# Performance work log

Hardware: AMD Instinct MI355X
Metric: run time of the kernel (lower is better)

The kernel has to match this reference:

```python
import jax, jax.numpy as jnp
import numpy as np

NUM_HEADS = 4
CHUNK = 64
GATE_NORM = 16.0
EPS = 1e-5


def _xavier(key, fan_in, fan_out):
    gain = 2.0 ** (-2.5)
    limit = gain * np.sqrt(6.0 / (fan_in + fan_out))
    return jax.random.uniform(key, (fan_in, fan_out), jnp.float32, -limit, limit)


def setup_inputs() -> dict:
    key = jax.random.key(0)
    ks = jax.random.split(key, 8)
    B, L, D = 4, 2048, 1024
    Dk, Dv, R = 1024, 2048, 16
    x = jax.random.normal(ks[0], (B, L, D), jnp.float32)
    return {
        "x": x,
        "Wq": _xavier(ks[1], D, Dk),
        "Wk": _xavier(ks[2], D, Dk),
        "Wv": _xavier(ks[3], D, Dv),
        "Wg": _xavier(ks[4], D, Dv),
        "gk_w1": _xavier(ks[5], D, R),
        "gk_w2": _xavier(ks[6], R, Dk),
        "gk_b2": jnp.zeros((Dk,), jnp.float32),
        "g_norm_w": jnp.ones((Dv // NUM_HEADS,), jnp.float32),
        "Wo": _xavier(ks[7], Dv, D),
    }


def _to_chunks(t, B, H, NC, C):
    # [B,H,L,d] -> [NC,B,H,C,d]
    d = t.shape[-1]
    return t.reshape(B, H, NC, C, d).transpose(2, 0, 1, 3, 4)


def _gla_forward(x, Wq, Wk, Wv, Wg, gk_w1, gk_w2, gk_b2, g_norm_w, Wo):
    B, L, D = x.shape
    H = NUM_HEADS
    C = CHUNK
    NC = L // C

    q = x @ Wq  # [B,L,Dk]
    k = x @ Wk
    v = x @ Wv  # [B,L,Dv]
    gk = jax.nn.log_sigmoid((x @ gk_w1) @ gk_w2 + gk_b2) / GATE_NORM  # [B,L,Dk]

    def split_heads(t):
        return t.reshape(B, L, H, -1).transpose(0, 2, 1, 3)  # [B,H,L,d]

    q, k, v, gk = map(split_heads, (q, k, v, gk))
    dk = q.shape[-1]
    scale = dk ** -0.5

    qc = _to_chunks(q, B, H, NC, C)
    kc = _to_chunks(k, B, H, NC, C)
    vc = _to_chunks(v, B, H, NC, C)
    gc = _to_chunks(gk, B, H, NC, C)
    Bcum = jnp.cumsum(gc, axis=3)  # inclusive log-decay within chunk

    causal = jnp.tril(jnp.ones((C, C), jnp.float32))  # s <= t

    def step(Hst, inp):
        qi, ki, vi, bi = inp  # [B,H,C,dk/dv]
        qg = qi * jnp.exp(bi) * scale           # q_t * exp(B_t)
        kg = ki * jnp.exp(-bi)                  # k_s * exp(-B_s)
        o_inter = jnp.einsum('bhcd,bhde->bhce', qg, Hst)
        A = jnp.einsum('bhtd,bhsd->bhts', qg, kg) * causal
        o_intra = jnp.einsum('bhts,bhse->bhte', A, vi)
        b_last = bi[:, :, -1:, :]               # total chunk decay [B,H,1,dk]
        kH = ki * jnp.exp(b_last - bi)          # decay remaining after s
        H_new = jnp.exp(b_last).transpose(0, 1, 3, 2) * Hst + \
            jnp.einsum('bhcd,bhce->bhde', kH, vi)
        return H_new, o_inter + o_intra

    dv = v.shape[-1]
    H0 = jnp.zeros((B, H, dk, dv), jnp.float32)
    _, oc = jax.lax.scan(step, H0, (qc, kc, vc, Bcum))  # [NC,B,H,C,dv]
    o = oc.transpose(1, 2, 0, 3, 4).reshape(B, H, L, dv)
    o = o.transpose(0, 2, 1, 3)  # [B,L,H,dv]

    # FusedRMSNormSwishGate: RMSNorm(o) * w * swish(g)
    rms = jnp.sqrt(jnp.mean(o * o, axis=-1, keepdims=True) + EPS)
    o_n = (o / rms) * g_norm_w
    g = (x @ Wg).reshape(B, L, H, dv)
    o = o_n * g * jax.nn.sigmoid(g)
    return o.reshape(B, L, H * dv) @ Wo


def reference(x, Wq, Wk, Wv, Wg, gk_w1, gk_w2, gk_b2, g_norm_w, Wo):
    return _gla_forward(x, Wq, Wk, Wv, Wg, gk_w1, gk_w2, gk_b2, g_norm_w, Wo)
```

## Files before the change

### kernel.cpp

```cpp
#include <hip/hip_runtime.h>
#include <hip/hip_bf16.h>

typedef __attribute__((ext_vector_type(8))) __bf16 bf16x8;
typedef __attribute__((ext_vector_type(4))) __bf16 bf16x4;
typedef __attribute__((ext_vector_type(4))) float f32x4;

#define MFMA16(a, b, c) __builtin_amdgcn_mfma_f32_16x16x32_bf16((a), (b), (c), 0, 0, 0)

__device__ __forceinline__ void gload_lds16(const void* g, void* l) {
    __builtin_amdgcn_global_load_lds((const __attribute__((address_space(1))) void*)g,
                                     (__attribute__((address_space(3))) void*)l, 16, 0, 0);
}

__device__ __forceinline__ int lds_swz(int r, int ck) {
    int W = ((r & 15) << 6) | (ck << 4);
    W ^= ((W >> 7) & 7) << 4;
    return ((r >> 4) << 9) + (W >> 1);
}

__global__ __launch_bounds__(256) void transpose_all(
    const float* __restrict__ Wq, const float* __restrict__ Wk,
    const float* __restrict__ Wg, const float* __restrict__ Wv,
    const float* __restrict__ Wo, __bf16* __restrict__ WTqk,
    __bf16* __restrict__ WTg, __bf16* __restrict__ WvT, __bf16* __restrict__ WoT) {
    __shared__ float tile[32][33];
    const int bid = blockIdx.x;
    const float* in;
    __bf16* out;
    int R, C, loc, gw;
    if (bid < 1024)      { in = Wq; out = WTqk;            R = 1024; C = 1024; loc = bid;        gw = 32; }
    else if (bid < 2048) { in = Wk; out = WTqk + 1048576;  R = 1024; C = 1024; loc = bid - 1024; gw = 32; }
    else if (bid < 4096) { in = Wg; out = WTg;             R = 1024; C = 2048; loc = bid - 2048; gw = 64; }
    else if (bid < 6144) { in = Wv; out = WvT;             R = 1024; C = 2048; loc = bid - 4096; gw = 64; }
    else                 { in = Wo; out = WoT;             R = 2048; C = 1024; loc = bid - 6144; gw = 32; }
    const int c0 = (loc % gw) * 32, r0 = (loc / gw) * 32;
    const int tx = threadIdx.x & 31, ty = threadIdx.x >> 5;
#pragma unroll
    for (int k = 0; k < 32; k += 8)
        tile[ty + k][tx] = in[(size_t)(r0 + ty + k) * C + c0 + tx];
    __syncthreads();
#pragma unroll
    for (int k = 0; k < 32; k += 8)
        out[(size_t)(c0 + ty + k) * R + r0 + tx] = (__bf16)tile[tx][ty + k];
}

template <typename OUT_T>
__global__ __launch_bounds__(256) void gemm_bt(const __bf16* __restrict__ A,
                                               const __bf16* __restrict__ Bt,
                                               OUT_T* __restrict__ C, int M, int N, int K) {
    __shared__ alignas(16) __bf16 As[2][4096];
    __shared__ alignas(16) __bf16 Bs[2][4096];
    const int tid = threadIdx.x;
    const int wv = tid >> 6;
    const int l = tid & 63;
    const int nwg = gridDim.x;
    const int cpx = nwg >> 3;
    const int bid = blockIdx.x;
    const int wg = (bid & 7) * cpx + (bid >> 3);
    const int nbn = N >> 7;
    const int bm = wg / nbn, bn = wg - bm * nbn;

    const __bf16* Ab = A + (size_t)bm * 128 * K;
    const __bf16* Bb = Bt + (size_t)bn * 128 * K;
    const int L = (l << 4) ^ ((l >> 3) << 4);
    const int sr = L >> 6;
    const int sc8 = ((L >> 4) & 3) * 8;
    const int lr = tid & 15;
    const int ck = (tid >> 4) & 3;
    const int wm = (wv >> 1) * 64, wn = (wv & 1) * 64;

    auto STAGE = [&](int buf, int kt) {
        gload_lds16(Ab + (size_t)(wv * 16 + sr) * K + kt + sc8, &As[buf][0] + wv * 512);
        gload_lds16(Ab + (size_t)(64 + wv * 16 + sr) * K + kt + sc8, &As[buf][0] + 2048 + wv * 512);
        gload_lds16(Bb + (size_t)(wv * 16 + sr) * K + kt + sc8, &Bs[buf][0] + wv * 512);
        gload_lds16(Bb + (size_t)(64 + wv * 16 + sr) * K + kt + sc8, &Bs[buf][0] + 2048 + wv * 512);
    };

    const int nt = K >> 5;
    STAGE(0, 0);

    f32x4 acc[4][4] = {};
    for (int t = 0; t < nt; ++t) {
        __builtin_amdgcn_s_barrier();
        __builtin_amdgcn_sched_barrier(0);
        if (t + 1 < nt) {
            STAGE((t + 1) & 1, (t + 1) * 32);
            asm volatile("s_waitcnt vmcnt(4)" ::: "memory");
        } else {
            asm volatile("s_waitcnt vmcnt(0)" ::: "memory");
        }
        __builtin_amdgcn_sched_barrier(0);
        const __bf16* as = &As[t & 1][0];
        const __bf16* bs = &Bs[t & 1][0];
        bf16x8 af[4], bfr[4];
#pragma unroll
        for (int i = 0; i < 4; i++) af[i] = *(const bf16x8*)(as + lds_swz(wm + i * 16 + lr, ck));
#pragma unroll
        for (int j = 0; j < 4; j++) bfr[j] = *(const bf16x8*)(bs + lds_swz(wn + j * 16 + lr, ck));
#pragma unroll
        for (int i = 0; i < 4; i++)
#pragma unroll
            for (int j = 0; j < 4; j++) acc[i][j] = MFMA16(af[i], bfr[j], acc[i][j]);
        asm volatile("s_waitcnt lgkmcnt(0)" ::: "memory");
    }
    const int lro = ((tid >> 4) & 3) * 4;
#pragma unroll
    for (int i = 0; i < 4; i++)
#pragma unroll
        for (int j = 0; j < 4; j++) {
            size_t base = (size_t)(bm * 128 + wm + i * 16 + lro) * N + bn * 128 + wn + j * 16 + lr;
#pragma unroll
            for (int r = 0; r < 4; r++) C[base + (size_t)r * N] = (OUT_T)acc[i][j][r];
        }
}

__global__ __launch_bounds__(256) void gemm_proj(const __bf16* __restrict__ xb,
                                                 const __bf16* __restrict__ WT,
                                                 const __bf16* __restrict__ WvT,
                                                 __bf16* __restrict__ Cq,
                                                 __bf16* __restrict__ Cg,
                                                 __bf16* __restrict__ vt) {
    constexpr int K = 1024;
    __shared__ alignas(16) __bf16 As[2][4096];
    __shared__ alignas(16) __bf16 Bs[2][4096];
    const int tid = threadIdx.x;
    const int wv = tid >> 6;
    const int l = tid & 63;
    const int bid = blockIdx.x;
    const int wg = (bid & 7) * 384 + (bid >> 3);
    const int mode = (wg >= 2048);
    int bm, bn;
    const __bf16 *Ab, *Bb;
    if (!mode) {
        bm = wg >> 5; bn = wg & 31;
        Ab = xb + (size_t)bm * 128 * K;
        Bb = WT + (size_t)bn * 128 * K;
    } else {
        const int w2 = wg - 2048;
        bm = w2 >> 6; bn = w2 & 63;
        Ab = WvT + (size_t)bm * 128 * K;
        Bb = xb + (size_t)bn * 128 * K;
    }
    const int L = (l << 4) ^ ((l >> 3) << 4);
    const int sr = L >> 6;
    const int sc8 = ((L >> 4) & 3) * 8;
    const int lr = tid & 15;
    const int ck = (tid >> 4) & 3;
    const int wm = (wv >> 1) * 64, wn = (wv & 1) * 64;

    auto STAGE = [&](int buf, int kt) {
        gload_lds16(Ab + (size_t)(wv * 16 + sr) * K + kt + sc8, &As[buf][0] + wv * 512);
        gload_lds16(Ab + (size_t)(64 + wv * 16 + sr) * K + kt + sc8, &As[buf][0] + 2048 + wv * 512);
        gload_lds16(Bb + (size_t)(wv * 16 + sr) * K + kt + sc8, &Bs[buf][0] + wv * 512);
        gload_lds16(Bb + (size_t)(64 + wv * 16 + sr) * K + kt + sc8, &Bs[buf][0] + 2048 + wv * 512);
    };

    const int nt = K >> 5;
    STAGE(0, 0);

    f32x4 acc[4][4] = {};
    for (int t = 0; t < nt; ++t) {
        __builtin_amdgcn_s_barrier();
        __builtin_amdgcn_sched_barrier(0);
        if (t + 1 < nt) {
            STAGE((t + 1) & 1, (t + 1) * 32);
            asm volatile("s_waitcnt vmcnt(4)" ::: "memory");
        } else {
            asm volatile("s_waitcnt vmcnt(0)" ::: "memory");
        }
        __builtin_amdgcn_sched_barrier(0);
        const __bf16* as = &As[t & 1][0];
        const __bf16* bs = &Bs[t & 1][0];
        bf16x8 af[4], bfr[4];
#pragma unroll
        for (int i = 0; i < 4; i++) af[i] = *(const bf16x8*)(as + lds_swz(wm + i * 16 + lr, ck));
#pragma unroll
        for (int j = 0; j < 4; j++) bfr[j] = *(const bf16x8*)(bs + lds_swz(wn + j * 16 + lr, ck));
#pragma unroll
        for (int i = 0; i < 4; i++)
#pragma unroll
            for (int j = 0; j < 4; j++) acc[i][j] = MFMA16(af[i], bfr[j], acc[i][j]);
        asm volatile("s_waitcnt lgkmcnt(0)" ::: "memory");
    }
    const int lro = ((tid >> 4) & 3) * 4;
    if (!mode) {
        __bf16* Cd = (bn < 16) ? Cq : Cg;
        const int col0 = (bn & 15) * 128;
#pragma unroll
        for (int i = 0; i < 4; i++)
#pragma unroll
            for (int j = 0; j < 4; j++) {
                size_t base = (size_t)(bm * 128 + wm + i * 16 + lro) * 2048 + col0 + wn + j * 16 + lr;
#pragma unroll
                for (int r = 0; r < 4; r++) Cd[base + (size_t)r * 2048] = (__bf16)acc[i][j][r];
            }
    } else {
#pragma unroll
        for (int i = 0; i < 4; i++)
#pragma unroll
            for (int j = 0; j < 4; j++) {
                size_t base = (size_t)(bm * 128 + wm + i * 16 + lro) * 8192 + bn * 128 + wn + j * 16 + lr;
#pragma unroll
                for (int r = 0; r < 4; r++) vt[base + (size_t)r * 8192] = (__bf16)acc[i][j][r];
            }
    }
}

__global__ __launch_bounds__(256) void gk1_cvt(const float* __restrict__ x,
                                               const float* __restrict__ w1,
                                               float* __restrict__ t,
                                               __bf16* __restrict__ xb) {
    const int row = blockIdx.x * 4 + (threadIdx.x >> 6);
    const int l = threadIdx.x & 63;
    const int r = l & 15, kg = l >> 4;
    const float* xr = x + (size_t)row * 1024;
    const float* w1p = w1 + r;
    float acc = 0.f;
    for (int k = kg * 256; k < (kg + 1) * 256; ++k) acc = fmaf(xr[k], w1p[k * 16], acc);
    acc += __shfl_xor(acc, 16);
    acc += __shfl_xor(acc, 32);
    if (kg == 0) t[(size_t)row * 16 + r] = acc;

    const size_t base = (size_t)blockIdx.x * 4096 + threadIdx.x * 16;
#pragma unroll
    for (int v = 0; v < 4; v++) {
        f32x4 f = *(const f32x4*)(x + base + v * 4);
        bf16x4 o;
#pragma unroll
        for (int j = 0; j < 4; j++) o[j] = (__bf16)f[j];
        *(bf16x4*)(xb + base + v * 4) = o;
    }
}

__global__ __launch_bounds__(1024, 4) void gate_qkg(
    const float* __restrict__ tbuf, const float* __restrict__ w2,
    const float* __restrict__ b2, const __bf16* __restrict__ qkbuf,
    __bf16* __restrict__ qg, __bf16* __restrict__ kg,
    __bf16* __restrict__ kgT, float* __restrict__ ebl) {
    __shared__ alignas(16) float t_l[128 * 16];
    __shared__ float qs[4 * 256];
    __shared__ __bf16 kg_l[128 * 260];
    const int bid = blockIdx.x;
    const int bh = bid & 15, nc = bid >> 4;
    const int b = bh >> 2, h = bh & 3;
    const int tid = threadIdx.x;
    const int d = tid & 255, cq = tid >> 8;
    const int seq0 = b * 2048 + nc * 128;
    const int hd = h * 256 + d;

    for (int i = tid; i < 128 * 16; i += 1024) t_l[i] = tbuf[(size_t)seq0 * 16 + i];
    float w2c[16];
#pragma unroll
    for (int r = 0; r < 16; r++) w2c[r] = w2[r * 1024 + hd];
    const float b2v = b2[hd];
    __syncthreads();

    float bs[32];
    float run = 0.f;
#pragma unroll
    for (int j = 0; j < 32; j++) {
        const int c = cq * 32 + j;
        f32x4 t0 = *(const f32x4*)(t_l + c * 16);
        f32x4 t1 = *(const f32x4*)(t_l + c * 16 + 4);
        f32x4 t2 = *(const f32x4*)(t_l + c * 16 + 8);
        f32x4 t3 = *(const f32x4*)(t_l + c * 16 + 12);
        float u = b2v;
#pragma unroll
        for (int r = 0; r < 4; r++) {
            u = fmaf(t0[r], w2c[r], u);
            u = fmaf(t1[r], w2c[4 + r], u);
            u = fmaf(t2[r], w2c[8 + r], u);
            u = fmaf(t3[r], w2c[12 + r], u);
        }
        const float ls = fminf(u, 0.f) - __logf(1.f + __expf(-fabsf(u)));
        run += ls * 0.0625f;
        bs[j] = run;
    }
    qs[cq * 256 + d] = run;
    __syncthreads();

    float prefix = 0.f;
#pragma unroll
    for (int q = 0; q < 3; q++)
        if (q < cq) prefix += qs[q * 256 + d];

#pragma unroll
    for (int j = 0; j < 32; j++) {
        const int c = cq * 32 + j;
        const float bsum = prefix + bs[j];
        const float eb = __expf(bsum);
        const float en = __expf(-bsum);
        const float qv = (float)qkbuf[(size_t)(seq0 + c) * 2048 + hd];
        const float kv = (float)qkbuf[(size_t)(seq0 + c) * 2048 + 1024 + hd];
        qg[(size_t)(seq0 + c) * 1024 + hd] = (__bf16)(qv * eb * 0.0625f);
        const __bf16 kgv = (__bf16)(kv * en);
        kg[(size_t)(seq0 + c) * 1024 + hd] = kgv;
        kg_l[c * 260 + d] = kgv;
    }
    if (cq == 3) ebl[(size_t)(nc * 16 + bh) * 256 + d] = __expf(prefix + bs[31]);
    __syncthreads();

    {
        const int cc = tid & 127, dgroup = tid >> 7;
        for (int i = 0; i < 32; i++) {
            const int dd = dgroup * 32 + i;
            kgT[(size_t)(bh * 256 + dd) * 2048 + nc * 128 + cc] = kg_l[cc * 260 + dd];
        }
    }
}

__global__ __launch_bounds__(512) void amat_chunku(
    const __bf16* __restrict__ qg, const __bf16* __restrict__ kg,
    __bf16* __restrict__ Abuf, const __bf16* __restrict__ vt,
    const __bf16* __restrict__ kgT, __bf16* __restrict__ UH) {
    const int tid = threadIdx.x, wv = tid >> 6, l = tid & 63;
    const int lr = l & 15, lk = (l >> 4) * 8, lro = (l >> 4) * 4;
    if (blockIdx.x < 256) {
        const int pair = blockIdx.x;
        const int bh = pair & 15, nc = pair >> 4;
        const int b = bh >> 2, h = bh & 3;
        const int seq0 = b * 2048 + nc * 128;
        __bf16* Ab = Abuf + (size_t)pair * 16384;
        {
            bf16x8 z = {};
            for (int i = tid; i < 2048; i += 512) *(bf16x8*)(Ab + (size_t)i * 8) = z;
        }
        __syncthreads();
        static const int TJ[36] = {0,1,1,2,2,2,3,3,3,3,4,4,4,4,4,5,5,5,5,5,5,
                                   6,6,6,6,6,6,6,7,7,7,7,7,7,7,7};
        static const int TS[36] = {0,0,1,0,1,2,0,1,2,3,0,1,2,3,4,0,1,2,3,4,5,
                                   0,1,2,3,4,5,6,0,1,2,3,4,5,6,7};
        for (int m = wv; m < 36; m += 8) {
            const int j = TJ[m], s = TS[m];
            f32x4 acc = {};
            const __bf16* qrow = qg + (size_t)(seq0 + j * 16 + lr) * 1024 + h * 256;
            const __bf16* krow = kg + (size_t)(seq0 + s * 16 + lr) * 1024 + h * 256;
#pragma unroll
            for (int ks = 0; ks < 8; ks++) {
                bf16x8 a = *(const bf16x8*)(qrow + ks * 32 + lk);
                bf16x8 bb = *(const bf16x8*)(krow + ks * 32 + lk);
                acc = MFMA16(a, bb, acc);
            }
#pragma unroll
            for (int r = 0; r < 4; r++) {
                const int t = j * 16 + lro + r;
                const int ss = s * 16 + lr;
                if (ss <= t) Ab[t * 128 + ss] = (__bf16)acc[r];
            }
        }
    } else {
        const int bid = blockIdx.x - 256;
        const int bh = bid & 15, nc = (bid >> 4) & 15, q = bid >> 8;
        const int eh = q >> 1, dh = q & 1;
        const int b = bh >> 2, h = bh & 3;
        const int seq0 = b * 2048 + nc * 128;
        const int e0 = eh * 256 + (wv >> 1) * 64;
        const int d0 = dh * 128 + (wv & 1) * 64;
        const __bf16* va = vt + (size_t)(h * 512 + e0) * 8192 + seq0;
        const __bf16* kb = kgT + (size_t)(bh * 256 + d0) * 2048 + nc * 128;

        f32x4 acc[4][4] = {};
#pragma unroll
        for (int ks = 0; ks < 4; ks++) {
            bf16x8 af[4], bf_[4];
#pragma unroll
            for (int i = 0; i < 4; i++)
                af[i] = *(const bf16x8*)(va + (size_t)(i * 16 + lr) * 8192 + ks * 32 + lk);
#pragma unroll
            for (int j = 0; j < 4; j++)
                bf_[j] = *(const bf16x8*)(kb + (size_t)(j * 16 + lr) * 2048 + ks * 32 + lk);
#pragma unroll
            for (int i = 0; i < 4; i++)
#pragma unroll
                for (int j = 0; j < 4; j++) acc[i][j] = MFMA16(af[i], bf_[j], acc[i][j]);
        }
        __bf16* ub = UH + ((size_t)(nc * 16 + bh) * 512 + e0) * 256 + d0;
#pragma unroll
        for (int i = 0; i < 4; i++)
#pragma unroll
            for (int j = 0; j < 4; j++)
#pragma unroll
                for (int r = 0; r < 4; r++)
                    ub[(size_t)(i * 16 + lro + r) * 256 + j * 16 + lr] = (__bf16)acc[i][j][r];
    }
}

__global__ __launch_bounds__(256) void ointer(
    const __bf16* __restrict__ Abuf, const __bf16* __restrict__ qg,
    const __bf16* __restrict__ vt, const __bf16* __restrict__ UH,
    __bf16* __restrict__ ob) {
    __shared__ alignas(16) __bf16 As[2][4096];
    __shared__ alignas(16) __bf16 Bs[2][4096];
    const int tid = threadIdx.x;
    const int wv = tid >> 6;
    const int l = tid & 63;
    const int bid = blockIdx.x;
    const int wg = (bid & 7) * 128 + (bid >> 3);
    const int bn = wg & 3, pair = wg >> 2;
    const int bh = pair & 15, nc = pair >> 4;
    const int b = bh >> 2, h = bh & 3;
    const int seq0 = b * 2048 + nc * 128;
    const int L = (l << 4) ^ ((l >> 3) << 4);
    const int sr = L >> 6;
    const int sc8 = ((L >> 4) & 3) * 8;
    const int lr = tid & 15;
    const int ck = (tid >> 4) & 3;
    const int wm = (wv >> 1) * 64, wn = (wv & 1) * 64;
    const int KE = (nc == 0) ? 128 : 384;

    const __bf16* Ap = Abuf + (size_t)pair * 16384;
    const __bf16* Hb = UH + ((size_t)((nc - 1) * 16 + bh) * 512 + bn * 128) * 256;

    auto STAGE = [&](int buf, int kt) {
        const __bf16 *a0, *a1, *b0, *b1;
        if (kt < 128) {
            a0 = Ap + (size_t)(wv * 16 + sr) * 128 + kt + sc8;
            a1 = Ap + (size_t)(64 + wv * 16 + sr) * 128 + kt + sc8;
            b0 = vt + (size_t)(h * 512 + bn * 128 + wv * 16 + sr) * 8192 + seq0 + kt + sc8;
            b1 = vt + (size_t)(h * 512 + bn * 128 + 64 + wv * 16 + sr) * 8192 + seq0 + kt + sc8;
        } else {
            const int kd = kt - 128;
            a0 = qg + (size_t)(seq0 + wv * 16 + sr) * 1024 + h * 256 + kd + sc8;
            a1 = qg + (size_t)(seq0 + 64 + wv * 16 + sr) * 1024 + h * 256 + kd + sc8;
            b0 = Hb + (size_t)(wv * 16 + sr) * 256 + kd + sc8;
            b1 = Hb + (size_t)(64 + wv * 16 + sr) * 256 + kd + sc8;
        }
        gload_lds16(a0, &As[buf][0] + wv * 512);
        gload_lds16(a1, &As[buf][0] + 2048 + wv * 512);
        gload_lds16(b0, &Bs[buf][0] + wv * 512);
        gload_lds16(b1, &Bs[buf][0] + 2048 + wv * 512);
    };

    const int nt = KE >> 5;
    STAGE(0, 0);

    f32x4 acc[4][4] = {};
    for (int t = 0; t < nt; ++t) {
        __builtin_amdgcn_s_barrier();
        __builtin_amdgcn_sched_barrier(0);
        if (t + 1 < nt) {
            STAGE((t + 1) & 1, (t + 1) * 32);
            asm volatile("s_waitcnt vmcnt(4)" ::: "memory");
        } else {
            asm volatile("s_waitcnt vmcnt(0)" ::: "memory");
        }
        __builtin_amdgcn_sched_barrier(0);
        const __bf16* as = &As[t & 1][0];
        const __bf16* bs = &Bs[t & 1][0];
        bf16x8 af[4], bfr[4];
#pragma unroll
        for (int i = 0; i < 4; i++) af[i] = *(const bf16x8*)(as + lds_swz(wm + i * 16 + lr, ck));
#pragma unroll
        for (int j = 0; j < 4; j++) bfr[j] = *(const bf16x8*)(bs + lds_swz(wn + j * 16 + lr, ck));
#pragma unroll
        for (int i = 0; i < 4; i++)
#pragma unroll
            for (int j = 0; j < 4; j++) acc[i][j] = MFMA16(af[i], bfr[j], acc[i][j]);
        asm volatile("s_waitcnt lgkmcnt(0)" ::: "memory");
    }
    const int lro = ((tid >> 4) & 3) * 4;
#pragma unroll
    for (int i = 0; i < 4; i++)
#pragma unroll
        for (int j = 0; j < 4; j++) {
            size_t base = (size_t)(seq0 + wm + i * 16 + lro) * 2048 + h * 512 + bn * 128 + wn + j * 16 + lr;
#pragma unroll
            for (int r = 0; r < 4; r++) ob[base + (size_t)r * 2048] = (__bf16)acc[i][j][r];
        }
}

__global__ __launch_bounds__(256) void hscan(__bf16* __restrict__ UH,
                                             const float* __restrict__ ebl) {
    const int t = blockIdx.x * 256 + threadIdx.x;
    const int bh = t >> 14;
    const int rem = t & 16383;
    const int e = rem >> 5, d0 = (rem & 31) * 8;
    float H[8];
#pragma unroll
    for (int j = 0; j < 8; j++) H[j] = 0.f;
    for (int i = 0; i < 16; i++) {
        size_t idx = ((size_t)(i * 16 + bh) * 512 + e) * 256 + d0;
        bf16x8 u = *(const bf16x8*)(UH + idx);
        const float* ep = ebl + (size_t)(i * 16 + bh) * 256 + d0;
        f32x4 e0v = *(const f32x4*)ep;
        f32x4 e1v = *(const f32x4*)(ep + 4);
        bf16x8 hw;
#pragma unroll
        for (int j = 0; j < 4; j++) {
            H[j] = e0v[j] * (H[j] + (float)u[j]);
            hw[j] = (__bf16)H[j];
        }
#pragma unroll
        for (int j = 4; j < 8; j++) {
            H[j] = e1v[j - 4] * (H[j] + (float)u[j]);
            hw[j] = (__bf16)H[j];
        }
        *(bf16x8*)(UH + idx) = hw;
    }
}

__global__ __launch_bounds__(256) void rms_gate(const __bf16* __restrict__ ob,
                                                const __bf16* __restrict__ gbuf,
                                                const float* __restrict__ gnw,
                                                __bf16* __restrict__ gated) {
    const int idx = blockIdx.x * 4 + (threadIdx.x >> 6);
    const int seq = idx >> 2, h = idx & 3;
    const int l = threadIdx.x & 63;
    bf16x8 o1 = *(const bf16x8*)(ob + (size_t)seq * 2048 + h * 512 + l * 8);
    float v[8];
    float ms = 0.f;
#pragma unroll
    for (int j = 0; j < 8; j++) {
        v[j] = (float)o1[j];
        ms += v[j] * v[j];
    }
#pragma unroll
    for (int off = 1; off < 64; off <<= 1) ms += __shfl_xor(ms, off);
    const float rinv = rsqrtf(ms * (1.f / 512.f) + 1e-5f);
    bf16x8 gv = *(const bf16x8*)(gbuf + (size_t)seq * 2048 + h * 512 + l * 8);
    const float* gw = gnw + l * 8;
    bf16x8 outv;
#pragma unroll
    for (int j = 0; j < 8; j++) {
        float g = (float)gv[j];
        float sig = 1.f / (1.f + expf(-g));
        outv[j] = (__bf16)(v[j] * rinv * gw[j] * g * sig);
    }
    *(bf16x8*)(gated + (size_t)seq * 2048 + h * 512 + l * 8) = outv;
}

extern "C" void kernel_launch(void* const* d_in, const int* in_sizes, int n_in,
                              void* d_out, int out_size, void* d_ws, size_t ws_size,
                              hipStream_t stream) {
    const float* x = (const float*)d_in[0];
    const float* Wq = (const float*)d_in[1];
    const float* Wk = (const float*)d_in[2];
    const float* Wv = (const float*)d_in[3];
    const float* Wg = (const float*)d_in[4];
    const float* w1 = (const float*)d_in[5];
    const float* w2 = (const float*)d_in[6];
    const float* b2 = (const float*)d_in[7];
    const float* gnw = (const float*)d_in[8];
    const float* Wo = (const float*)d_in[9];
    float* out = (float*)d_out;

    char* p = (char*)d_ws;
    auto nxt = [&](size_t bytes) {
        char* r = p;
        p += (bytes + 255) & ~(size_t)255;
        return r;
    };
    __bf16* xb = (__bf16*)nxt(8192ull * 1024 * 2);
    __bf16* WTqk = (__bf16*)nxt(2048ull * 1024 * 2);
    __bf16* WTg = (__bf16*)nxt(2048ull * 1024 * 2);
    __bf16* WvT = (__bf16*)nxt(2048ull * 1024 * 2);
    __bf16* WoT = (__bf16*)nxt(1024ull * 2048 * 2);
    __bf16* gbuf = (__bf16*)nxt(8192ull * 2048 * 2);
    __bf16* vt = (__bf16*)nxt(2048ull * 8192 * 2);
    float* tbuf = (float*)nxt(8192ull * 16 * 4);
    __bf16* qg = (__bf16*)nxt(8192ull * 1024 * 2);
    __bf16* kgT = (__bf16*)nxt(16ull * 256 * 2048 * 2);
    float* ebl = (float*)nxt(16ull * 16 * 256 * 4);
    __bf16* ob = (__bf16*)nxt(8192ull * 2048 * 2);
    __bf16* UH = (__bf16*)nxt(16ull * 16 * 512 * 256 * 2);
    __bf16* kg = xb;
    __bf16* qkbuf = UH;
    __bf16* gated = UH;
    __bf16* Abuf = WTqk;

    gk1_cvt<<<2048, 256, 0, stream>>>(x, w1, tbuf, xb);
    transpose_all<<<8192, 256, 0, stream>>>(Wq, Wk, Wg, Wv, Wo, WTqk, WTg, WvT, WoT);
    gemm_proj<<<3072, 256, 0, stream>>>(xb, WTqk, WvT, qkbuf, gbuf, vt);
    gate_qkg<<<256, 1024, 0, stream>>>(tbuf, w2, b2, qkbuf, qg, kg, kgT, ebl);
    amat_chunku<<<1280, 512, 0, stream>>>(qg, kg, Abuf, vt, kgT, UH);
    hscan<<<1024, 256, 0, stream>>>(UH, ebl);
    ointer<<<1024, 256, 0, stream>>>(Abuf, qg, vt, UH, ob);
    rms_gate<<<8192, 256, 0, stream>>>(ob, gbuf, gnw, gated);
    gemm_bt<float><<<512, 256, 0, stream>>>(gated, WoT, out, 8192, 1024, 2048);
}
```

Baseline: 377.5 us.

## Split-K output GEMM with atomics and merge prep kernels into one launch

The final Wo projection now uses a split-K GEMM. K=2048 is divided into two halves, giving 1024 workgroups instead of 512 and better CU occupancy, and partial sums are combined with float atomicAdd into a zeroed output. The gk1/convert kernel and the weight transpose kernel are merged into a single prep launch to save one launch gap. This costs an extra memset and atomic write traffic to the output, and the order of floating-point accumulation becomes nondeterministic.

```diff
diff --git a/kernel.cpp b/kernel.cpp
--- a/kernel.cpp
+++ b/kernel.cpp
@@ -18,13 +18,38 @@
     return ((r >> 4) << 9) + (W >> 1);
 }
 
-__global__ __launch_bounds__(256) void transpose_all(
+__global__ __launch_bounds__(256) void prep(
+    const float* __restrict__ x, const float* __restrict__ w1,
+    float* __restrict__ t, __bf16* __restrict__ xb,
     const float* __restrict__ Wq, const float* __restrict__ Wk,
     const float* __restrict__ Wg, const float* __restrict__ Wv,
     const float* __restrict__ Wo, __bf16* __restrict__ WTqk,
     __bf16* __restrict__ WTg, __bf16* __restrict__ WvT, __bf16* __restrict__ WoT) {
     __shared__ float tile[32][33];
-    const int bid = blockIdx.x;
+    if (blockIdx.x < 2048) {
+        const int row = blockIdx.x * 4 + (threadIdx.x >> 6);
+        const int l = threadIdx.x & 63;
+        const int r = l & 15, kg = l >> 4;
+        const float* xr = x + (size_t)row * 1024;
+        const float* w1p = w1 + r;
+        float acc = 0.f;
+        for (int k = kg * 256; k < (kg + 1) * 256; ++k) acc = fmaf(xr[k], w1p[k * 16], acc);
+        acc += __shfl_xor(acc, 16);
+        acc += __shfl_xor(acc, 32);
+        if (kg == 0) t[(size_t)row * 16 + r] = acc;
+
+        const size_t base = (size_t)blockIdx.x * 4096 + threadIdx.x * 16;
+#pragma unroll
+        for (int v = 0; v < 4; v++) {
+            f32x4 f = *(const f32x4*)(x + base + v * 4);
+            bf16x4 o;
+#pragma unroll
+            for (int j = 0; j < 4; j++) o[j] = (__bf16)f[j];
+            *(bf16x4*)(xb + base + v * 4) = o;
+        }
+        return;
+    }
+    const int bid = blockIdx.x - 2048;
     const float* in;
     __bf16* out;
     int R, C, loc, gw;
@@ -42,76 +67,6 @@
 #pragma unroll
     for (int k = 0; k < 32; k += 8)
         out[(size_t)(c0 + ty + k) * R + r0 + tx] = (__bf16)tile[tx][ty + k];
-}
-
-template <typename OUT_T>
-__global__ __launch_bounds__(256) void gemm_bt(const __bf16* __restrict__ A,
-                                               const __bf16* __restrict__ Bt,
-                                               OUT_T* __restrict__ C, int M, int N, int K) {
-    __shared__ alignas(16) __bf16 As[2][4096];
-    __shared__ alignas(16) __bf16 Bs[2][4096];
-    const int tid = threadIdx.x;
-    const int wv = tid >> 6;
-    const int l = tid & 63;
-    const int nwg = gridDim.x;
-    const int cpx = nwg >> 3;
-    const int bid = blockIdx.x;
-    const int wg = (bid & 7) * cpx + (bid >> 3);
-    const int nbn = N >> 7;
-    const int bm = wg / nbn, bn = wg - bm * nbn;
-
-    const __bf16* Ab = A + (size_t)bm * 128 * K;
-    const __bf16* Bb = Bt + (size_t)bn * 128 * K;
-    const int L = (l << 4) ^ ((l >> 3) << 4);
-    const int sr = L >> 6;
-    const int sc8 = ((L >> 4) & 3) * 8;
-    const int lr = tid & 15;
-    const int ck = (tid >> 4) & 3;
-    const int wm = (wv >> 1) * 64, wn = (wv & 1) * 64;
-
-    auto STAGE = [&](int buf, int kt) {
-        gload_lds16(Ab + (size_t)(wv * 16 + sr) * K + kt + sc8, &As[buf][0] + wv * 512);
-        gload_lds16(Ab + (size_t)(64 + wv * 16 + sr) * K + kt + sc8, &As[buf][0] + 2048 + wv * 512);
-        gload_lds16(Bb + (size_t)(wv * 16 + sr) * K + kt + sc8, &Bs[buf][0] + wv * 512);
-        gload_lds16(Bb + (size_t)(64 + wv * 16 + sr) * K + kt + sc8, &Bs[buf][0] + 2048 + wv * 512);
-    };
-
-    const int nt = K >> 5;
-    STAGE(0, 0);
-
-    f32x4 acc[4][4] = {};
-    for (int t = 0; t < nt; ++t) {
-        __builtin_amdgcn_s_barrier();
-        __builtin_amdgcn_sched_barrier(0);
-        if (t + 1 < nt) {
-            STAGE((t + 1) & 1, (t + 1) * 32);
-            asm volatile("s_waitcnt vmcnt(4)" ::: "memory");
-        } else {
-            asm volatile("s_waitcnt vmcnt(0)" ::: "memory");
-        }
-        __builtin_amdgcn_sched_barrier(0);
-        const __bf16* as = &As[t & 1][0];
-        const __bf16* bs = &Bs[t & 1][0];
-        bf16x8 af[4], bfr[4];
-#pragma unroll
-        for (int i = 0; i < 4; i++) af[i] = *(const bf16x8*)(as + lds_swz(wm + i * 16 + lr, ck));
-#pragma unroll
-        for (int j = 0; j < 4; j++) bfr[j] = *(const bf16x8*)(bs + lds_swz(wn + j * 16 + lr, ck));
-#pragma unroll
-        for (int i = 0; i < 4; i++)
-#pragma unroll
-            for (int j = 0; j < 4; j++) acc[i][j] = MFMA16(af[i], bfr[j], acc[i][j]);
-        asm volatile("s_waitcnt lgkmcnt(0)" ::: "memory");
-    }
-    const int lro = ((tid >> 4) & 3) * 4;
-#pragma unroll
-    for (int i = 0; i < 4; i++)
-#pragma unroll
-        for (int j = 0; j < 4; j++) {
-            size_t base = (size_t)(bm * 128 + wm + i * 16 + lro) * N + bn * 128 + wn + j * 16 + lr;
-#pragma unroll
-            for (int r = 0; r < 4; r++) C[base + (size_t)r * N] = (OUT_T)acc[i][j][r];
-        }
 }
 
 __global__ __launch_bounds__(256) void gemm_proj(const __bf16* __restrict__ xb,
@@ -206,30 +161,72 @@
     }
 }
 
-__global__ __launch_bounds__(256) void gk1_cvt(const float* __restrict__ x,
-                                               const float* __restrict__ w1,
-                                               float* __restrict__ t,
-                                               __bf16* __restrict__ xb) {
-    const int row = blockIdx.x * 4 + (threadIdx.x >> 6);
-    const int l = threadIdx.x & 63;
-    const int r = l & 15, kg = l >> 4;
-    const float* xr = x + (size_t)row * 1024;
-    const float* w1p = w1 + r;
-    float acc = 0.f;
-    for (int k = kg * 256; k < (kg + 1) * 256; ++k) acc = fmaf(xr[k], w1p[k * 16], acc);
-    acc += __shfl_xor(acc, 16);
-    acc += __shfl_xor(acc, 32);
-    if (kg == 0) t[(size_t)row * 16 + r] = acc;
-
-    const size_t base = (size_t)blockIdx.x * 4096 + threadIdx.x * 16;
-#pragma unroll
-    for (int v = 0; v < 4; v++) {
-        f32x4 f = *(const f32x4*)(x + base + v * 4);
-        bf16x4 o;
-#pragma unroll
-        for (int j = 0; j < 4; j++) o[j] = (__bf16)f[j];
-        *(bf16x4*)(xb + base + v * 4) = o;
-    }
+__global__ __launch_bounds__(256) void gemm_wo(const __bf16* __restrict__ A,
+                                               const __bf16* __restrict__ Bt,
+                                               float* __restrict__ C) {
+    constexpr int K = 2048, KH = 1024, N = 1024;
+    __shared__ alignas(16) __bf16 As[2][4096];
+    __shared__ alignas(16) __bf16 Bs[2][4096];
+    const int tid = threadIdx.x;
+    const int wv = tid >> 6;
+    const int l = tid & 63;
+    const int bid = blockIdx.x;
+    const int wg = (bid & 7) * 128 + (bid >> 3);
+    const int kh = wg >> 9, tile = wg & 511;
+    const int bm = tile >> 3, bn = tile & 7;
+
+    const __bf16* Ab = A + (size_t)bm * 128 * K + kh * KH;
+    const __bf16* Bb = Bt + (size_t)bn * 128 * K + kh * KH;
+    const int L = (l << 4) ^ ((l >> 3) << 4);
+    const int sr = L >> 6;
+    const int sc8 = ((L >> 4) & 3) * 8;
+    const int lr = tid & 15;
+    const int ck = (tid >> 4) & 3;
+    const int wm = (wv >> 1) * 64, wn = (wv & 1) * 64;
+
+    auto STAGE = [&](int buf, int kt) {
+        gload_lds16(Ab + (size_t)(wv * 16 + sr) * K + kt + sc8, &As[buf][0] + wv * 512);
+        gload_lds16(Ab + (size_t)(64 + wv * 16 + sr) * K + kt + sc8, &As[buf][0] + 2048 + wv * 512);
+        gload_lds16(Bb + (size_t)(wv * 16 + sr) * K + kt + sc8, &Bs[buf][0] + wv * 512);
+        gload_lds16(Bb + (size_t)(64 + wv * 16 + sr) * K + kt + sc8, &Bs[buf][0] + 2048 + wv * 512);
+    };
+
+    const int nt = KH >> 5;
+    STAGE(0, 0);
+
+    f32x4 acc[4][4] = {};
+    for (int t = 0; t < nt; ++t) {
+        __builtin_amdgcn_s_barrier();
+        __builtin_amdgcn_sched_barrier(0);
+        if (t + 1 < nt) {
+            STAGE((t + 1) & 1, (t + 1) * 32);
+            asm volatile("s_waitcnt vmcnt(4)" ::: "memory");
+        } else {
+            asm volatile("s_waitcnt vmcnt(0)" ::: "memory");
+        }
+        __builtin_amdgcn_sched_barrier(0);
+        const __bf16* as = &As[t & 1][0];
+        const __bf16* bs = &Bs[t & 1][0];
+        bf16x8 af[4], bfr[4];
+#pragma unroll
+        for (int i = 0; i < 4; i++) af[i] = *(const bf16x8*)(as + lds_swz(wm + i * 16 + lr, ck));
+#pragma unroll
+        for (int j = 0; j < 4; j++) bfr[j] = *(const bf16x8*)(bs + lds_swz(wn + j * 16 + lr, ck));
+#pragma unroll
+        for (int i = 0; i < 4; i++)
+#pragma unroll
+            for (int j = 0; j < 4; j++) acc[i][j] = MFMA16(af[i], bfr[j], acc[i][j]);
+        asm volatile("s_waitcnt lgkmcnt(0)" ::: "memory");
+    }
+    const int lro = ((tid >> 4) & 3) * 4;
+#pragma unroll
+    for (int i = 0; i < 4; i++)
+#pragma unroll
+        for (int j = 0; j < 4; j++) {
+            size_t base = (size_t)(bm * 128 + wm + i * 16 + lro) * N + bn * 128 + wn + j * 16 + lr;
+#pragma unroll
+            for (int r = 0; r < 4; r++) atomicAdd(&C[base + (size_t)r * N], acc[i][j][r]);
+        }
 }
 
 __global__ __launch_bounds__(1024, 4) void gate_qkg(
@@ -568,13 +565,13 @@
     __bf16* gated = UH;
     __bf16* Abuf = WTqk;
 
-    gk1_cvt<<<2048, 256, 0, stream>>>(x, w1, tbuf, xb);
-    transpose_all<<<8192, 256, 0, stream>>>(Wq, Wk, Wg, Wv, Wo, WTqk, WTg, WvT, WoT);
+    prep<<<10240, 256, 0, stream>>>(x, w1, tbuf, xb, Wq, Wk, Wg, Wv, Wo, WTqk, WTg, WvT, WoT);
     gemm_proj<<<3072, 256, 0, stream>>>(xb, WTqk, WvT, qkbuf, gbuf, vt);
     gate_qkg<<<256, 1024, 0, stream>>>(tbuf, w2, b2, qkbuf, qg, kg, kgT, ebl);
     amat_chunku<<<1280, 512, 0, stream>>>(qg, kg, Abuf, vt, kgT, UH);
     hscan<<<1024, 256, 0, stream>>>(UH, ebl);
     ointer<<<1024, 256, 0, stream>>>(Abuf, qg, vt, UH, ob);
     rms_gate<<<8192, 256, 0, stream>>>(ob, gbuf, gnw, gated);
-    gemm_bt<float><<<512, 256, 0, stream>>>(gated, WoT, out, 8192, 1024, 2048);
-}
+    hipMemsetAsync(out, 0, 8192ull * 1024 * 4, stream);
+    gemm_wo<<<1024, 256, 0, stream>>>(gated, WoT, out);
+}
```

Measured after the change: 414.6 us. +9.8%, slower.
